# Performance work log

Hardware: AMD Instinct MI355X
Metric: run time of the kernel (lower is better)

Reference implementation:

```python
import jax, jax.numpy as jnp
import numpy as np

B, N, D, H, K = 32, 100, 4, 256, 4  # batch, num_vars, input_size, n_hid, num_edge_types
SKIP_FIRST = True


def _edge_indices(n):
    e = np.ones((n, n)) - np.eye(n)
    s, r = np.where(e)
    return jnp.asarray(s, jnp.int32), jnp.asarray(r, jnp.int32)


def setup_inputs() -> dict:
    key = jax.random.key(0)
    ks = jax.random.split(key, 24)
    E = N * (N - 1)
    send, recv = _edge_indices(N)
    w = lambda k, shape: jax.random.normal(k, shape, jnp.float32) * 0.05
    b = lambda shape: jnp.full(shape, 0.1, jnp.float32)
    return {
        'inputs': jax.random.normal(ks[0], (B, N, D), jnp.float32),
        'hidden': jax.random.normal(ks[1], (B, N, H), jnp.float32),
        'edges': jax.random.uniform(ks[2], (B, E, K), jnp.float32),
        'msg_W1': w(ks[3], (K, 2 * H, H)), 'msg_b1': b((K, H)),
        'msg_W2': w(ks[4], (K, H, H)), 'msg_b2': b((K, H)),
        'Whr': w(ks[5], (H, H)), 'Whi': w(ks[6], (H, H)), 'Whh': w(ks[7], (H, H)),
        'Wir': w(ks[8], (D, H)), 'bir': b((H,)),
        'Wii': w(ks[9], (D, H)), 'bii': b((H,)),
        'Win': w(ks[10], (D, H)), 'bin_': b((H,)),
        'Wo1': w(ks[11], (H, H)), 'bo1': b((H,)),
        'Wo2': w(ks[12], (H, H)), 'bo2': b((H,)),
        'Wo3': w(ks[13], (H, D)), 'bo3': b((D,)),
        'send_edges': send, 'recv_edges': recv,
    }


def reference(inputs, hidden, edges, msg_W1, msg_b1, msg_W2, msg_b2,
              Whr, Whi, Whh, Wir, bir, Wii, bii, Win, bin_,
              Wo1, bo1, Wo2, bo2, Wo3, bo3, send_edges, recv_edges):
    # gather sender/receiver hidden states -> [B, E, 2H]
    pre_msg = jnp.concatenate([hidden[:, recv_edges], hidden[:, send_edges]], axis=-1)
    start = 1 if SKIP_FIRST else 0
    norm = float(K - 1) if SKIP_FIRST else float(K)
    all_msgs = jnp.zeros(pre_msg.shape[:2] + (H,), pre_msg.dtype)
    for i in range(start, K):  # fixed small loop over edge types
        m = jnp.tanh(pre_msg @ msg_W1[i] + msg_b1[i])
        m = jnp.tanh(m @ msg_W2[i] + msg_b2[i])
        all_msgs = all_msgs + m * edges[:, :, i:i + 1] / norm
    # scatter-sum messages to receiver nodes (== edge2node one-hot matmul)
    agg = jnp.zeros_like(hidden).at[:, recv_edges].add(all_msgs) / (N - 1)
    # GRU-style fused update
    r = jax.nn.sigmoid(inputs @ Wir + bir + agg @ Whr)
    i_g = jax.nn.sigmoid(inputs @ Wii + bii + agg @ Whi)
    n = jnp.tanh(inputs @ Win + bin_ + r * (agg @ Whh))
    hidden_new = (1.0 - i_g) * n + i_g * hidden
    # output MLP with residual (dropout p=0 in eval)
    pred = jax.nn.relu(hidden_new @ Wo1 + bo1)
    pred = jax.nn.relu(pred @ Wo2 + bo2)
    pred = inputs + (pred @ Wo3 + bo3)
    return pred, hidden_new
```

## Files before the change

kernel.cpp:

```cpp
#include <hip/hip_runtime.h>
#include <hip/hip_bf16.h>


typedef __attribute__((ext_vector_type(4))) float f32x4;
typedef __attribute__((ext_vector_type(8))) short s16x8;
typedef __attribute__((ext_vector_type(4))) unsigned short u16x4;
typedef __attribute__((ext_vector_type(4))) unsigned int u32x4;
typedef __attribute__((ext_vector_type(2))) unsigned int u32x2;

#define DEV static __device__ __forceinline__

DEV unsigned short f2bf(float f) {
  unsigned int u = __builtin_bit_cast(unsigned int, f);
  u += 0x7fffu + ((u >> 16) & 1u);
  return (unsigned short)(u >> 16);
}
DEV float bf2f(unsigned short h) {
  unsigned int u = ((unsigned int)h) << 16;
  return __builtin_bit_cast(float, u);
}
DEV float bflo(unsigned int u) { return __builtin_bit_cast(float, u << 16); }
DEV float bfhi(unsigned int u) { return __builtin_bit_cast(float, u & 0xffff0000u); }
DEV float exp2_fast(float x) { return __builtin_amdgcn_exp2f(x); }
DEV float tanh_fast(float x) {
  float e = exp2_fast(x * 2.885390082f);
  return 1.f - 2.f * __builtin_amdgcn_rcpf(e + 1.f);
}
DEV float sigmoid_fast(float x) {
  return __builtin_amdgcn_rcpf(1.f + exp2_fast(-1.442695041f * x));
}
DEV unsigned int pk_fp8x4(float a, float b, float c, float d) {
  int v = __builtin_amdgcn_cvt_pk_fp8_f32(a, b, 0, false);
  v = __builtin_amdgcn_cvt_pk_fp8_f32(c, d, v, true);
  return (unsigned int)v;
}
DEV void gload_lds16(const unsigned char* g, unsigned char* l) {
  __builtin_amdgcn_global_load_lds(
      (const __attribute__((address_space(1))) void*)g,
      (__attribute__((address_space(3))) void*)l, 16, 0, 0);
}

DEV void stage_bf16_64(const unsigned short* __restrict__ src, unsigned char* smem, int tid) {
#pragma unroll
  for (int j = 0; j < 8; ++j) {
    int c = tid + 256 * j;
    int s = c >> 5, hc = c & 31;
    s16x8 v = *reinterpret_cast<const s16x8*>(src + s * 256 + hc * 8);
    int byte = (s * 512 + hc * 16) ^ ((s & 7) << 4);
    *reinterpret_cast<s16x8*>(smem + byte) = v;
  }
}
DEV void stage_f32_64(const float* __restrict__ src, unsigned char* smem, int tid) {
#pragma unroll
  for (int j = 0; j < 8; ++j) {
    int c = tid + 256 * j;
    int s = c >> 5, hc = c & 31;
    const float* p = src + s * 256 + hc * 8;
    f32x4 v0 = *reinterpret_cast<const f32x4*>(p);
    f32x4 v1 = *reinterpret_cast<const f32x4*>(p + 4);
    s16x8 o;
#pragma unroll
    for (int i = 0; i < 4; ++i) { o[i] = (short)f2bf(v0[i]); o[4 + i] = (short)f2bf(v1[i]); }
    int byte = (s * 512 + hc * 16) ^ ((s & 7) << 4);
    *reinterpret_cast<s16x8*>(smem + byte) = o;
  }
}
DEV void stage_sum3_f32(const float* __restrict__ sa, const float* __restrict__ sb,
                        const float* __restrict__ sc, unsigned char* smem, int tid) {
#pragma unroll
  for (int j = 0; j < 8; ++j) {
    int c = tid + 256 * j;
    int s = c >> 5, hc = c & 31;
    int o4 = s * 256 + hc * 8;
    f32x4 a0 = *reinterpret_cast<const f32x4*>(sa + o4);
    f32x4 a1 = *reinterpret_cast<const f32x4*>(sa + o4 + 4);
    f32x4 b0 = *reinterpret_cast<const f32x4*>(sb + o4);
    f32x4 b1 = *reinterpret_cast<const f32x4*>(sb + o4 + 4);
    f32x4 c0 = *reinterpret_cast<const f32x4*>(sc + o4);
    f32x4 c1 = *reinterpret_cast<const f32x4*>(sc + o4 + 4);
    s16x8 o;
#pragma unroll
    for (int i = 0; i < 4; ++i) {
      o[i] = (short)f2bf(a0[i] + b0[i] + c0[i]);
      o[4 + i] = (short)f2bf(a1[i] + b1[i] + c1[i]);
    }
    int byte = (s * 512 + hc * 16) ^ ((s & 7) << 4);
    *reinterpret_cast<s16x8*>(smem + byte) = o;
  }
}

template<int MF>
DEV void gemm_lds_tile(const unsigned char* smemA, const unsigned short* __restrict__ B,
                       int nb, int lane, f32x4 acc[][4]) {
  int li = lane & 15, lg = lane >> 4;
#pragma unroll
  for (int kk = 0; kk < 8; ++kk) {
    int kb = kk * 32 + lg * 8;
    s16x8 a[MF];
#pragma unroll
    for (int m = 0; m < MF; ++m) {
      int row = m * 16 + li;
      int byte = (row * 512 + kb * 2) ^ ((row & 7) << 4);
      a[m] = *reinterpret_cast<const s16x8*>(smemA + byte);
    }
#pragma unroll
    for (int n = 0; n < 4; ++n) {
      int col = nb + n * 16 + li;
      s16x8 bf = *reinterpret_cast<const s16x8*>(B + col * 256 + kb);
#pragma unroll
      for (int m = 0; m < MF; ++m)
        acc[m][n] = __builtin_amdgcn_mfma_f32_16x16x32_bf16(a[m], bf, acc[m][n], 0, 0, 0);
    }
  }
}

__global__ __launch_bounds__(256) void k0_pack(
    const float* __restrict__ msg_W1,
    const float* __restrict__ Whr, const float* __restrict__ Whi, const float* __restrict__ Whh,
    const float* __restrict__ Wo1, const float* __restrict__ Wo2,
    unsigned short* __restrict__ W1aT, unsigned short* __restrict__ W1bT,
    unsigned short* __restrict__ WhT) {
  int g = blockIdx.x * 256 + threadIdx.x;
  if (g < 196608) {
    int ti = g >> 16, rem = g & 65535, n = rem >> 8, k = rem & 255;
    W1aT[g] = f2bf(msg_W1[((ti + 1) * 512 + k) * 256 + n]);
  } else if (g < 393216) {
    int h = g - 196608; int ti = h >> 16, rem = h & 65535, n = rem >> 8, k = rem & 255;
    W1bT[h] = f2bf(msg_W1[((ti + 1) * 512 + 256 + k) * 256 + n]);
  } else if (g < 720896) {
    int h = g - 393216; int mi = h >> 16, rem = h & 65535, n = rem >> 8, k = rem & 255;
    const float* s = mi == 0 ? Whr : mi == 1 ? Whi : mi == 2 ? Whh : mi == 3 ? Wo1 : Wo2;
    WhT[h] = f2bf(s[k * 256 + n]);
  }
}

__global__ __launch_bounds__(256) void k0_quant(
    const float* __restrict__ msg_W2, unsigned short* __restrict__ W2Q) {
  int g = blockIdx.x * 256 + threadIdx.x;
  int ti = g >> 15, rem = g & 32767, col = rem >> 7, k2 = rem & 127;
  int k = k2 * 2;
  const float* src = msg_W2 + (size_t)(ti + 1) * 65536;
  float a = src[k * 256 + col], b = src[(k + 1) * 256 + col];
  int v = __builtin_amdgcn_cvt_pk_fp8_f32(a, b, 0, false);
  W2Q[g] = (unsigned short)(v & 0xffff);
}

__global__ __launch_bounds__(256) void k_xpre(
    const float* __restrict__ inputs, const float* __restrict__ Wir, const float* __restrict__ bir,
    const float* __restrict__ Wii, const float* __restrict__ bii,
    const float* __restrict__ Win, const float* __restrict__ bin_, float* __restrict__ Xpre) {
  int g = blockIdx.x * 256 + threadIdx.x;
  int row = g / 768, c = g % 768, which = c >> 8, col = c & 255;
  const float* W = which == 0 ? Wir : which == 1 ? Wii : Win;
  const float* bb = which == 0 ? bir : which == 1 ? bii : bin_;
  const float* inp = inputs + row * 4;
  float s = bb[col];
#pragma unroll
  for (int d = 0; d < 4; ++d) s += inp[d] * W[d * 256 + col];
  Xpre[g] = s;
}

__global__ __launch_bounds__(256) void k1_nodepre(
    const float* __restrict__ hidden, const float* __restrict__ msg_b1,
    const unsigned short* __restrict__ W1aT, const unsigned short* __restrict__ W1bT,
    unsigned short* __restrict__ Ha, unsigned short* __restrict__ Hb) {
  __shared__ alignas(16) unsigned char smem[32768];
  int tid = threadIdx.x, lane = tid & 63, wv = tid >> 6;
  int mt = blockIdx.x, g = blockIdx.y;
  stage_f32_64(hidden + (size_t)mt * 64 * 256, smem, tid);
  __syncthreads();
  int ti = g < 3 ? g : g - 3;
  const unsigned short* Bp = (g < 3 ? W1aT : W1bT) + ti * 65536;
  f32x4 zz = {0.f, 0.f, 0.f, 0.f};
  f32x4 acc[4][4];
#pragma unroll
  for (int m = 0; m < 4; ++m)
#pragma unroll
    for (int n = 0; n < 4; ++n) acc[m][n] = zz;
  gemm_lds_tile<4>(smem, Bp, wv * 64, lane, acc);
  unsigned short* dst = (g < 3 ? Ha : Hb) + (size_t)ti * 819200 + (size_t)mt * 64 * 256;
  int li = lane & 15, lg = lane >> 4;
#pragma unroll
  for (int n = 0; n < 4; ++n) {
    int col = wv * 64 + n * 16 + li;
    float bias = g < 3 ? msg_b1[(ti + 1) * 256 + col] : 0.f;
#pragma unroll
    for (int m = 0; m < 4; ++m)
#pragma unroll
      for (int q = 0; q < 4; ++q) {
        int row = m * 16 + lg * 4 + q;
        dst[row * 256 + col] = f2bf(acc[m][n][q] + bias);
      }
  }
}

__global__ __launch_bounds__(256) void k2a_build(
    const unsigned short* __restrict__ Ha, const unsigned short* __restrict__ Hb,
    unsigned char* __restrict__ m1G, int ti) {
  int tid = threadIdx.x;
  int bid0 = blockIdx.x;
  int bid = (bid0 & 7) * 400 + (bid0 >> 3);
  int b = bid / 100, r = bid % 100;
  int hc = tid & 31, srow0 = tid >> 5;

  u32x4 hau = *reinterpret_cast<const u32x4*>(
      Ha + ((size_t)ti * 3200 + b * 100 + r) * 256 + hc * 8);
  float ha_f[8];
#pragma unroll
  for (int i = 0; i < 4; ++i) { ha_f[2 * i] = bflo(hau[i]); ha_f[2 * i + 1] = bfhi(hau[i]); }
  const unsigned short* HbB = Hb + ((size_t)ti * 3200 + b * 100) * 256;
  unsigned char* dst = m1G + (size_t)bid * 28672;
#pragma unroll
  for (int j = 0; j < 14; ++j) {
    int s = srow0 + 8 * j;
    u32x2 o = {0u, 0u};
    if (s < 99) {
      int snode = s + (s >= r ? 1 : 0);
      u32x4 hb = *reinterpret_cast<const u32x4*>(HbB + snode * 256 + hc * 8);
      float t[8];
#pragma unroll
      for (int i = 0; i < 4; ++i) {
        t[2 * i] = tanh_fast(ha_f[2 * i] + bflo(hb[i]));
        t[2 * i + 1] = tanh_fast(ha_f[2 * i + 1] + bfhi(hb[i]));
      }
      o[0] = pk_fp8x4(t[0], t[1], t[2], t[3]);
      o[1] = pk_fp8x4(t[4], t[5], t[6], t[7]);
    }
    int byte = (s * 256 + hc * 8) ^ ((s & 7) << 4);
    *reinterpret_cast<u32x2*>(dst + byte) = o;
  }
}

__global__ __launch_bounds__(256) void k2b_gemm(
    const float* __restrict__ edges, const float* __restrict__ msg_b2,
    const unsigned char* __restrict__ m1G, const unsigned char* __restrict__ W2Q,
    float* __restrict__ pagg, int ti) {
  __shared__ alignas(16) unsigned char smem[30144];
  float* w_s = (float*)(smem + 28672);
  float* agg_s = (float*)(smem + 29120);
  int tid = threadIdx.x, lane = tid & 63, wv = tid >> 6;
  int li = lane & 15, lg = lane >> 4;
  int bid0 = blockIdx.x;
  int bid = (bid0 & 7) * 400 + (bid0 >> 3);
  int b = bid / 100, r = bid % 100;

  const unsigned char* src = m1G + (size_t)bid * 28672;
#pragma unroll
  for (int j = 0; j < 7; ++j) {
    int chunk = wv * 7 + j;
    gload_lds16(src + chunk * 1024 + lane * 16, smem + chunk * 1024);
  }
  {
    float w0 = 0.f;
    if (tid < 99) {
      int snode = tid + (tid >= r ? 1 : 0);
      int e = snode * 99 + r - (r > snode ? 1 : 0);
      w0 = edges[(size_t)(b * 9900 + e) * 4 + (ti + 1)] * (1.f / 297.f);
    }
    if (tid < 112) w_s[tid] = w0;
  }
  __syncthreads();

  float b2r[4];
#pragma unroll
  for (int n = 0; n < 4; ++n)
    b2r[n] = msg_b2[(ti + 1) * 256 + wv * 64 + n * 16 + li];

  float aggacc[4] = {0.f, 0.f, 0.f, 0.f};
  f32x4 zz = {0.f, 0.f, 0.f, 0.f};
  const unsigned char* Bq = W2Q + (size_t)ti * 65536;
#pragma unroll
  for (int p = 0; p < 2; ++p) {
    f32x4 acc[7][2];
#pragma unroll
    for (int m = 0; m < 7; ++m) { acc[m][0] = zz; acc[m][1] = zz; }
#pragma unroll
    for (int kk = 0; kk < 8; ++kk) {
      int ko = kk * 32 + lg * 8;
      long a[7];
#pragma unroll
      for (int m = 0; m < 7; ++m) {
        int row = m * 16 + li;
        int byte = (row * 256 + ko) ^ ((row & 7) << 4);
        a[m] = *reinterpret_cast<const long*>(smem + byte);
      }
#pragma unroll
      for (int n = 0; n < 2; ++n) {
        int col = wv * 64 + p * 32 + n * 16 + li;
        long bq = *reinterpret_cast<const long*>(Bq + col * 256 + ko);
#pragma unroll
        for (int m = 0; m < 7; ++m)
          acc[m][n] = __builtin_amdgcn_mfma_f32_16x16x32_fp8_fp8(a[m], bq, acc[m][n], 0, 0, 0);
      }
    }
#pragma unroll
    for (int n = 0; n < 2; ++n) {
      float b2v = b2r[p * 2 + n];
      float pa = 0.f;
#pragma unroll
      for (int m = 0; m < 7; ++m) {
        f32x4 wf = *reinterpret_cast<const f32x4*>(w_s + m * 16 + lg * 4);
#pragma unroll
        for (int q = 0; q < 4; ++q)
          pa += tanh_fast(acc[m][n][q] + b2v) * wf[q];
      }
      aggacc[p * 2 + n] += pa;
    }
  }

#pragma unroll
  for (int n = 0; n < 4; ++n) {
    float v = aggacc[n];
    v += __shfl_xor(v, 16);
    v += __shfl_xor(v, 32);
    if (lane < 16) agg_s[wv * 64 + n * 16 + lane] = v;
  }
  __syncthreads();
  pagg[(size_t)ti * 819200 + (size_t)bid * 256 + tid] = agg_s[tid];
}

__global__ __launch_bounds__(256) void k3_gemm(
    const float* __restrict__ pagg, const unsigned short* __restrict__ WhT,
    float* __restrict__ RIH) {
  __shared__ alignas(16) unsigned char smem[32768];
  int tid = threadIdx.x, lane = tid & 63, wv = tid >> 6;
  int mt = blockIdx.x, y = blockIdx.y;
  size_t base = (size_t)mt * 64 * 256;
  stage_sum3_f32(pagg + base, pagg + 819200 + base, pagg + 1638400 + base, smem, tid);
  __syncthreads();
  f32x4 zz = {0.f, 0.f, 0.f, 0.f};
  f32x4 acc[4][4];
#pragma unroll
  for (int m = 0; m < 4; ++m)
#pragma unroll
    for (int n = 0; n < 4; ++n) acc[m][n] = zz;
  gemm_lds_tile<4>(smem, WhT + y * 65536, wv * 64, lane, acc);
  float* dst = RIH + (size_t)y * 819200 + base;
  int li = lane & 15, lg = lane >> 4;
#pragma unroll
  for (int n = 0; n < 4; ++n) {
    int col = wv * 64 + n * 16 + li;
#pragma unroll
    for (int m = 0; m < 4; ++m)
#pragma unroll
      for (int q = 0; q < 4; ++q)
        dst[(m * 16 + lg * 4 + q) * 256 + col] = acc[m][n][q];
  }
}

__global__ __launch_bounds__(256) void k4_gru(
    const float* __restrict__ Xpre, const float* __restrict__ RIH,
    const float* __restrict__ hidden, float* __restrict__ out, unsigned short* __restrict__ hnewbf) {
  int idx = blockIdx.x * 256 + threadIdx.x;
  int row = idx >> 8, col = idx & 255;
  float xr = Xpre[row * 768 + col];
  float xi = Xpre[row * 768 + 256 + col];
  float xn = Xpre[row * 768 + 512 + col];
  float rr = sigmoid_fast(xr + RIH[idx]);
  float ig = sigmoid_fast(xi + RIH[819200 + idx]);
  float nn = tanh_fast(xn + rr * RIH[1638400 + idx]);
  float hn = (1.f - ig) * nn + ig * hidden[idx];
  out[12800 + idx] = hn;
  hnewbf[idx] = f2bf(hn);
}

__global__ __launch_bounds__(256) void k_mlp(
    const unsigned short* __restrict__ A, const unsigned short* __restrict__ WT,
    const float* __restrict__ bias, unsigned short* __restrict__ dst) {
  __shared__ alignas(16) unsigned char smem[32768];
  int tid = threadIdx.x, lane = tid & 63, wv = tid >> 6;
  int mt = blockIdx.x;
  stage_bf16_64(A + (size_t)mt * 64 * 256, smem, tid);
  __syncthreads();
  f32x4 zz = {0.f, 0.f, 0.f, 0.f};
  f32x4 acc[4][4];
#pragma unroll
  for (int m = 0; m < 4; ++m)
#pragma unroll
    for (int n = 0; n < 4; ++n) acc[m][n] = zz;
  gemm_lds_tile<4>(smem, WT, wv * 64, lane, acc);
  unsigned short* d = dst + (size_t)mt * 64 * 256;
  int li = lane & 15, lg = lane >> 4;
#pragma unroll
  for (int n = 0; n < 4; ++n) {
    int col = wv * 64 + n * 16 + li;
    float bv = bias[col];
#pragma unroll
    for (int m = 0; m < 4; ++m)
#pragma unroll
      for (int q = 0; q < 4; ++q) {
        float v = fmaxf(acc[m][n][q] + bv, 0.f);
        d[(m * 16 + lg * 4 + q) * 256 + col] = f2bf(v);
      }
  }
}

__global__ __launch_bounds__(64) void k7_out(
    const unsigned short* __restrict__ pred2, const float* __restrict__ Wo3,
    const float* __restrict__ bo3, const float* __restrict__ inputs, float* __restrict__ out) {
  int row = blockIdx.x, lane = threadIdx.x;
  u16x4 p = *reinterpret_cast<const u16x4*>(pred2 + (size_t)row * 256 + lane * 4);
  float s0 = 0.f, s1 = 0.f, s2 = 0.f, s3 = 0.f;
#pragma unroll
  for (int j = 0; j < 4; ++j) {
    float pv = bf2f(p[j]);
    const float* wr = Wo3 + (lane * 4 + j) * 4;
    s0 += pv * wr[0]; s1 += pv * wr[1]; s2 += pv * wr[2]; s3 += pv * wr[3];
  }
#pragma unroll
  for (int off = 32; off >= 1; off >>= 1) {
    s0 += __shfl_xor(s0, off); s1 += __shfl_xor(s1, off);
    s2 += __shfl_xor(s2, off); s3 += __shfl_xor(s3, off);
  }
  if (lane == 0) {
    out[row * 4 + 0] = inputs[row * 4 + 0] + s0 + bo3[0];
    out[row * 4 + 1] = inputs[row * 4 + 1] + s1 + bo3[1];
    out[row * 4 + 2] = inputs[row * 4 + 2] + s2 + bo3[2];
    out[row * 4 + 3] = inputs[row * 4 + 3] + s3 + bo3[3];
  }
}

extern "C" void kernel_launch(void* const* d_in, const int* in_sizes, int n_in,
                              void* d_out, int out_size, void* d_ws, size_t ws_size,
                              hipStream_t stream) {
  const float* inputs = (const float*)d_in[0];
  const float* hidden = (const float*)d_in[1];
  const float* edges  = (const float*)d_in[2];
  const float* msg_W1 = (const float*)d_in[3];
  const float* msg_b1 = (const float*)d_in[4];
  const float* msg_W2 = (const float*)d_in[5];
  const float* msg_b2 = (const float*)d_in[6];
  const float* Whr = (const float*)d_in[7];
  const float* Whi = (const float*)d_in[8];
  const float* Whh = (const float*)d_in[9];
  const float* Wir = (const float*)d_in[10];
  const float* bir = (const float*)d_in[11];
  const float* Wii = (const float*)d_in[12];
  const float* bii = (const float*)d_in[13];
  const float* Win = (const float*)d_in[14];
  const float* bin_ = (const float*)d_in[15];
  const float* Wo1 = (const float*)d_in[16];
  const float* bo1 = (const float*)d_in[17];
  const float* Wo2 = (const float*)d_in[18];
  const float* bo2 = (const float*)d_in[19];
  const float* Wo3 = (const float*)d_in[20];
  const float* bo3 = (const float*)d_in[21];
  float* out = (float*)d_out;

  char* ws = (char*)d_ws;
  size_t off = 0;
  auto take = [&](size_t bytes) -> char* {
    char* p = ws + off;
    off += (bytes + 511) & ~(size_t)511;
    return p;
  };
  unsigned short* W1aT = (unsigned short*)take(196608 * 2);
  unsigned short* W1bT = (unsigned short*)take(196608 * 2);
  unsigned short* W2Q  = (unsigned short*)take(196608);
  unsigned short* WhT  = (unsigned short*)take(327680 * 2);
  unsigned short* Ha   = (unsigned short*)take(2457600 * 2);
  unsigned short* Hb   = (unsigned short*)take(2457600 * 2);
  float* pagg = (float*)take(3 * 819200 * 4);
  unsigned char* m1G = (unsigned char*)take((size_t)3200 * 28672);
  float* Xpre = (float*)take(2457600 * 4);
  float* RIH  = (float*)take(2457600 * 4);
  unsigned short* hnewbf = (unsigned short*)take(819200 * 2);
  unsigned short* pred1  = (unsigned short*)take(819200 * 2);
  unsigned short* pred2  = (unsigned short*)take(819200 * 2);

  k0_pack<<<2816, 256, 0, stream>>>(msg_W1, Whr, Whi, Whh, Wo1, Wo2, W1aT, W1bT, WhT);
  k0_quant<<<384, 256, 0, stream>>>(msg_W2, W2Q);
  k_xpre<<<9600, 256, 0, stream>>>(inputs, Wir, bir, Wii, bii, Win, bin_, Xpre);
  k1_nodepre<<<dim3(50, 6), 256, 0, stream>>>(hidden, msg_b1, W1aT, W1bT, Ha, Hb);
  for (int ti = 0; ti < 3; ++ti) {
    k2a_build<<<3200, 256, 0, stream>>>(Ha, Hb, m1G, ti);
    k2b_gemm<<<3200, 256, 0, stream>>>(edges, msg_b2, m1G,
                                       (const unsigned char*)W2Q, pagg, ti);
  }
  k3_gemm<<<dim3(50, 3), 256, 0, stream>>>(pagg, WhT, RIH);
  k4_gru<<<3200, 256, 0, stream>>>(Xpre, RIH, hidden, out, hnewbf);
  k_mlp<<<50, 256, 0, stream>>>(hnewbf, WhT + 196608, bo1, pred1);
  k_mlp<<<50, 256, 0, stream>>>(pred1, WhT + 262144, bo2, pred2);
  k7_out<<<3200, 64, 0, stream>>>(pred2, Wo3, bo3, inputs, out);
}
```

Measured before the change: 356.3 us.

## Split node GEMMs across more blocks and merge weight-prep kernels into one launch

Three preprocessing kernels (weight pack, W2 fp8 quantisation, input projection) are merged into a single launch dispatched by block index. The node-level GEMM kernels (k1_nodepre, k3_gemm, k_mlp) now also split the output columns across a grid dimension, so each wave computes fewer column tiles. Launching 2x or 4x more blocks should fill far more of the GPU's compute units than the previous 50–300-block grids. The cost is that each extra block re-stages the same A tile into LDS, and the merged kernel adds per-block branching.

```diff
diff --git a/kernel.cpp b/kernel.cpp
--- a/kernel.cpp
+++ b/kernel.cpp
@@ -89,9 +89,9 @@
   }
 }
 
-template<int MF>
-DEV void gemm_lds_tile(const unsigned char* smemA, const unsigned short* __restrict__ B,
-                       int nb, int lane, f32x4 acc[][4]) {
+template<int MF, int NF>
+DEV void gemm_tile(const unsigned char* smemA, const unsigned short* __restrict__ B,
+                   int nb, int lane, f32x4 acc[MF][NF]) {
   int li = lane & 15, lg = lane >> 4;
 #pragma unroll
   for (int kk = 0; kk < 8; ++kk) {
@@ -104,7 +104,7 @@
       a[m] = *reinterpret_cast<const s16x8*>(smemA + byte);
     }
 #pragma unroll
-    for (int n = 0; n < 4; ++n) {
+    for (int n = 0; n < NF; ++n) {
       int col = nb + n * 16 + li;
       s16x8 bf = *reinterpret_cast<const s16x8*>(B + col * 256 + kb);
 #pragma unroll
@@ -114,50 +114,49 @@
   }
 }
 
-__global__ __launch_bounds__(256) void k0_pack(
-    const float* __restrict__ msg_W1,
+__global__ __launch_bounds__(256) void kpre(
+    const float* __restrict__ msg_W1, const float* __restrict__ msg_W2,
     const float* __restrict__ Whr, const float* __restrict__ Whi, const float* __restrict__ Whh,
     const float* __restrict__ Wo1, const float* __restrict__ Wo2,
-    unsigned short* __restrict__ W1aT, unsigned short* __restrict__ W1bT,
-    unsigned short* __restrict__ WhT) {
-  int g = blockIdx.x * 256 + threadIdx.x;
-  if (g < 196608) {
-    int ti = g >> 16, rem = g & 65535, n = rem >> 8, k = rem & 255;
-    W1aT[g] = f2bf(msg_W1[((ti + 1) * 512 + k) * 256 + n]);
-  } else if (g < 393216) {
-    int h = g - 196608; int ti = h >> 16, rem = h & 65535, n = rem >> 8, k = rem & 255;
-    W1bT[h] = f2bf(msg_W1[((ti + 1) * 512 + 256 + k) * 256 + n]);
-  } else if (g < 720896) {
-    int h = g - 393216; int mi = h >> 16, rem = h & 65535, n = rem >> 8, k = rem & 255;
-    const float* s = mi == 0 ? Whr : mi == 1 ? Whi : mi == 2 ? Whh : mi == 3 ? Wo1 : Wo2;
-    WhT[h] = f2bf(s[k * 256 + n]);
-  }
-}
-
-__global__ __launch_bounds__(256) void k0_quant(
-    const float* __restrict__ msg_W2, unsigned short* __restrict__ W2Q) {
-  int g = blockIdx.x * 256 + threadIdx.x;
-  int ti = g >> 15, rem = g & 32767, col = rem >> 7, k2 = rem & 127;
-  int k = k2 * 2;
-  const float* src = msg_W2 + (size_t)(ti + 1) * 65536;
-  float a = src[k * 256 + col], b = src[(k + 1) * 256 + col];
-  int v = __builtin_amdgcn_cvt_pk_fp8_f32(a, b, 0, false);
-  W2Q[g] = (unsigned short)(v & 0xffff);
-}
-
-__global__ __launch_bounds__(256) void k_xpre(
     const float* __restrict__ inputs, const float* __restrict__ Wir, const float* __restrict__ bir,
     const float* __restrict__ Wii, const float* __restrict__ bii,
-    const float* __restrict__ Win, const float* __restrict__ bin_, float* __restrict__ Xpre) {
-  int g = blockIdx.x * 256 + threadIdx.x;
-  int row = g / 768, c = g % 768, which = c >> 8, col = c & 255;
-  const float* W = which == 0 ? Wir : which == 1 ? Wii : Win;
-  const float* bb = which == 0 ? bir : which == 1 ? bii : bin_;
-  const float* inp = inputs + row * 4;
-  float s = bb[col];
-#pragma unroll
-  for (int d = 0; d < 4; ++d) s += inp[d] * W[d * 256 + col];
-  Xpre[g] = s;
+    const float* __restrict__ Win, const float* __restrict__ bin_,
+    unsigned short* __restrict__ W1aT, unsigned short* __restrict__ W1bT,
+    unsigned short* __restrict__ WhT, unsigned short* __restrict__ W2Q,
+    float* __restrict__ Xpre) {
+  int blk = blockIdx.x, tid = threadIdx.x;
+  if (blk < 2816) {
+    int g = blk * 256 + tid;
+    if (g < 196608) {
+      int ti = g >> 16, rem = g & 65535, n = rem >> 8, k = rem & 255;
+      W1aT[g] = f2bf(msg_W1[((ti + 1) * 512 + k) * 256 + n]);
+    } else if (g < 393216) {
+      int h = g - 196608; int ti = h >> 16, rem = h & 65535, n = rem >> 8, k = rem & 255;
+      W1bT[h] = f2bf(msg_W1[((ti + 1) * 512 + 256 + k) * 256 + n]);
+    } else if (g < 720896) {
+      int h = g - 393216; int mi = h >> 16, rem = h & 65535, n = rem >> 8, k = rem & 255;
+      const float* s = mi == 0 ? Whr : mi == 1 ? Whi : mi == 2 ? Whh : mi == 3 ? Wo1 : Wo2;
+      WhT[h] = f2bf(s[k * 256 + n]);
+    }
+  } else if (blk < 3200) {
+    int g = (blk - 2816) * 256 + tid;
+    int ti = g >> 15, rem = g & 32767, col = rem >> 7, k2 = rem & 127;
+    int k = k2 * 2;
+    const float* src = msg_W2 + (size_t)(ti + 1) * 65536;
+    float a = src[k * 256 + col], b = src[(k + 1) * 256 + col];
+    int v = __builtin_amdgcn_cvt_pk_fp8_f32(a, b, 0, false);
+    W2Q[g] = (unsigned short)(v & 0xffff);
+  } else {
+    int g = (blk - 3200) * 256 + tid;
+    int row = g / 768, c = g % 768, which = c >> 8, col = c & 255;
+    const float* W = which == 0 ? Wir : which == 1 ? Wii : Win;
+    const float* bb = which == 0 ? bir : which == 1 ? bii : bin_;
+    const float* inp = inputs + row * 4;
+    float s = bb[col];
+#pragma unroll
+    for (int d = 0; d < 4; ++d) s += inp[d] * W[d * 256 + col];
+    Xpre[g] = s;
+  }
 }
 
 __global__ __launch_bounds__(256) void k1_nodepre(
@@ -166,23 +165,22 @@
     unsigned short* __restrict__ Ha, unsigned short* __restrict__ Hb) {
   __shared__ alignas(16) unsigned char smem[32768];
   int tid = threadIdx.x, lane = tid & 63, wv = tid >> 6;
-  int mt = blockIdx.x, g = blockIdx.y;
+  int mt = blockIdx.x, g = blockIdx.y, z = blockIdx.z;
   stage_f32_64(hidden + (size_t)mt * 64 * 256, smem, tid);
   __syncthreads();
   int ti = g < 3 ? g : g - 3;
   const unsigned short* Bp = (g < 3 ? W1aT : W1bT) + ti * 65536;
+  int nb = z * 128 + wv * 32;
   f32x4 zz = {0.f, 0.f, 0.f, 0.f};
-  f32x4 acc[4][4];
-#pragma unroll
-  for (int m = 0; m < 4; ++m)
-#pragma unroll
-    for (int n = 0; n < 4; ++n) acc[m][n] = zz;
-  gemm_lds_tile<4>(smem, Bp, wv * 64, lane, acc);
+  f32x4 acc[4][2];
+#pragma unroll
+  for (int m = 0; m < 4; ++m) { acc[m][0] = zz; acc[m][1] = zz; }
+  gemm_tile<4, 2>(smem, Bp, nb, lane, acc);
   unsigned short* dst = (g < 3 ? Ha : Hb) + (size_t)ti * 819200 + (size_t)mt * 64 * 256;
   int li = lane & 15, lg = lane >> 4;
 #pragma unroll
-  for (int n = 0; n < 4; ++n) {
-    int col = wv * 64 + n * 16 + li;
+  for (int n = 0; n < 2; ++n) {
+    int col = nb + n * 16 + li;
     float bias = g < 3 ? msg_b1[(ti + 1) * 256 + col] : 0.f;
 #pragma unroll
     for (int m = 0; m < 4; ++m)
@@ -324,22 +322,21 @@
     float* __restrict__ RIH) {
   __shared__ alignas(16) unsigned char smem[32768];
   int tid = threadIdx.x, lane = tid & 63, wv = tid >> 6;
-  int mt = blockIdx.x, y = blockIdx.y;
+  int mt = blockIdx.x, y = blockIdx.y, z = blockIdx.z;
   size_t base = (size_t)mt * 64 * 256;
   stage_sum3_f32(pagg + base, pagg + 819200 + base, pagg + 1638400 + base, smem, tid);
   __syncthreads();
+  int nb = z * 128 + wv * 32;
   f32x4 zz = {0.f, 0.f, 0.f, 0.f};
-  f32x4 acc[4][4];
-#pragma unroll
-  for (int m = 0; m < 4; ++m)
-#pragma unroll
-    for (int n = 0; n < 4; ++n) acc[m][n] = zz;
-  gemm_lds_tile<4>(smem, WhT + y * 65536, wv * 64, lane, acc);
+  f32x4 acc[4][2];
+#pragma unroll
+  for (int m = 0; m < 4; ++m) { acc[m][0] = zz; acc[m][1] = zz; }
+  gemm_tile<4, 2>(smem, WhT + y * 65536, nb, lane, acc);
   float* dst = RIH + (size_t)y * 819200 + base;
   int li = lane & 15, lg = lane >> 4;
 #pragma unroll
-  for (int n = 0; n < 4; ++n) {
-    int col = wv * 64 + n * 16 + li;
+  for (int n = 0; n < 2; ++n) {
+    int col = nb + n * 16 + li;
 #pragma unroll
     for (int m = 0; m < 4; ++m)
 #pragma unroll
@@ -369,30 +366,26 @@
     const float* __restrict__ bias, unsigned short* __restrict__ dst) {
   __shared__ alignas(16) unsigned char smem[32768];
   int tid = threadIdx.x, lane = tid & 63, wv = tid >> 6;
-  int mt = blockIdx.x;
+  int mt = blockIdx.x, y = blockIdx.y;
   stage_bf16_64(A + (size_t)mt * 64 * 256, smem, tid);
   __syncthreads();
+  int nb = y * 64 + wv * 16;
   f32x4 zz = {0.f, 0.f, 0.f, 0.f};
-  f32x4 acc[4][4];
-#pragma unroll
-  for (int m = 0; m < 4; ++m)
-#pragma unroll
-    for (int n = 0; n < 4; ++n) acc[m][n] = zz;
-  gemm_lds_tile<4>(smem, WT, wv * 64, lane, acc);
+  f32x4 acc[4][1];
+#pragma unroll
+  for (int m = 0; m < 4; ++m) acc[m][0] = zz;
+  gemm_tile<4, 1>(smem, WT, nb, lane, acc);
   unsigned short* d = dst + (size_t)mt * 64 * 256;
   int li = lane & 15, lg = lane >> 4;
-#pragma unroll
-  for (int n = 0; n < 4; ++n) {
-    int col = wv * 64 + n * 16 + li;
-    float bv = bias[col];
-#pragma unroll
-    for (int m = 0; m < 4; ++m)
-#pragma unroll
-      for (int q = 0; q < 4; ++q) {
-        float v = fmaxf(acc[m][n][q] + bv, 0.f);
-        d[(m * 16 + lg * 4 + q) * 256 + col] = f2bf(v);
-      }
-  }
+  int col = nb + li;
+  float bv = bias[col];
+#pragma unroll
+  for (int m = 0; m < 4; ++m)
+#pragma unroll
+    for (int q = 0; q < 4; ++q) {
+      float v = fmaxf(acc[m][0][q] + bv, 0.f);
+      d[(m * 16 + lg * 4 + q) * 256 + col] = f2bf(v);
+    }
 }
 
 __global__ __launch_bounds__(64) void k7_out(
@@ -468,18 +461,18 @@
   unsigned short* pred1  = (unsigned short*)take(819200 * 2);
   unsigned short* pred2  = (unsigned short*)take(819200 * 2);
 
-  k0_pack<<<2816, 256, 0, stream>>>(msg_W1, Whr, Whi, Whh, Wo1, Wo2, W1aT, W1bT, WhT);
-  k0_quant<<<384, 256, 0, stream>>>(msg_W2, W2Q);
-  k_xpre<<<9600, 256, 0, stream>>>(inputs, Wir, bir, Wii, bii, Win, bin_, Xpre);
-  k1_nodepre<<<dim3(50, 6), 256, 0, stream>>>(hidden, msg_b1, W1aT, W1bT, Ha, Hb);
+  kpre<<<12800, 256, 0, stream>>>(msg_W1, msg_W2, Whr, Whi, Whh, Wo1, Wo2,
+                                  inputs, Wir, bir, Wii, bii, Win, bin_,
+                                  W1aT, W1bT, WhT, W2Q, Xpre);
+  k1_nodepre<<<dim3(50, 6, 2), 256, 0, stream>>>(hidden, msg_b1, W1aT, W1bT, Ha, Hb);
   for (int ti = 0; ti < 3; ++ti) {
     k2a_build<<<3200, 256, 0, stream>>>(Ha, Hb, m1G, ti);
     k2b_gemm<<<3200, 256, 0, stream>>>(edges, msg_b2, m1G,
                                        (const unsigned char*)W2Q, pagg, ti);
   }
-  k3_gemm<<<dim3(50, 3), 256, 0, stream>>>(pagg, WhT, RIH);
+  k3_gemm<<<dim3(50, 3, 2), 256, 0, stream>>>(pagg, WhT, RIH);
   k4_gru<<<3200, 256, 0, stream>>>(Xpre, RIH, hidden, out, hnewbf);
-  k_mlp<<<50, 256, 0, stream>>>(hnewbf, WhT + 196608, bo1, pred1);
-  k_mlp<<<50, 256, 0, stream>>>(pred1, WhT + 262144, bo2, pred2);
+  k_mlp<<<dim3(50, 4), 256, 0, stream>>>(hnewbf, WhT + 196608, bo1, pred1);
+  k_mlp<<<dim3(50, 4), 256, 0, stream>>>(pred1, WhT + 262144, bo2, pred2);
   k7_out<<<3200, 64, 0, stream>>>(pred2, Wo3, bo3, inputs, out);
 }
```

New measurement: 333.9 us. 1.07x faster.
